# Optimization experiments

Measured on AMD Instinct MI355X. Metric: run time of the kernel, lower is better.

## Reference

```python
import jax, jax.numpy as jnp
import numpy as np

N_HEADS = 12

def setup_inputs() -> dict:
    key = jax.random.key(0)
    ks = jax.random.split(key, 5)
    B, T, H = 8, 1024, 768
    x = jax.random.normal(ks[0], (B, T, H), dtype=jnp.float32)
    # PyTorch Linear init: U(-1/sqrt(fan_in), 1/sqrt(fan_in))
    s1 = 1.0 / np.sqrt(H)
    W_attn = jax.random.uniform(ks[1], (H, 3 * H), minval=-s1, maxval=s1, dtype=jnp.float32)
    b_attn = jax.random.uniform(ks[2], (3 * H,), minval=-s1, maxval=s1, dtype=jnp.float32)
    W_proj = jax.random.uniform(ks[3], (H, H), minval=-s1, maxval=s1, dtype=jnp.float32)
    b_proj = jax.random.uniform(ks[4], (H,), minval=-s1, maxval=s1, dtype=jnp.float32)
    return {"x": x, "W_attn": W_attn, "b_attn": b_attn, "W_proj": W_proj, "b_proj": b_proj}

def reference(x, W_attn, b_attn, W_proj, b_proj):
    B, T, H = x.shape
    nh = N_HEADS
    Hs = H // nh
    qkv = x @ W_attn + b_attn                       # [B,T,3H]
    q, k, v = jnp.split(qkv, 3, axis=-1)            # each [B,T,H]
    # -> [B, nh, T, Hs]
    q = q.reshape(B, T, nh, Hs).transpose(0, 2, 1, 3)
    k = k.reshape(B, T, nh, Hs).transpose(0, 2, 1, 3)
    v = v.reshape(B, T, nh, Hs).transpose(0, 2, 1, 3)
    scale = 1.0 / jnp.sqrt(jnp.asarray(Hs, dtype=x.dtype))
    scores = jnp.einsum("bhqd,bhkd->bhqk", q, k) * scale  # [B,nh,T,T]
    causal = jnp.tril(jnp.ones((T, T), dtype=bool))
    scores = jnp.where(causal, scores, jnp.asarray(-jnp.inf, dtype=scores.dtype))
    attn = jax.nn.softmax(scores, axis=-1)
    out = jnp.einsum("bhqk,bhkd->bhqd", attn, v)    # [B,nh,T,Hs]
    out = out.transpose(0, 2, 1, 3).reshape(B, T, H)
    return out @ W_proj + b_proj
```

## Files before the change

kernel.cpp:

```cpp
#include <hip/hip_runtime.h>
#include <hip/hip_bf16.h>
#include <math.h>


typedef __attribute__((ext_vector_type(4))) float  f32x4;
typedef __attribute__((ext_vector_type(8))) short  bf16x8;
typedef __attribute__((ext_vector_type(4))) short  bf16x4;
typedef __attribute__((ext_vector_type(4))) unsigned int u32x4;

__device__ __forceinline__ unsigned short f2bf(float f) {
    union { float f; unsigned u; } v; v.f = f;
    unsigned r = (v.u + 0x7FFFu + ((v.u >> 16) & 1u)) >> 16;
    return (unsigned short)r;
}

__device__ __forceinline__ bf16x4 pk4(float a, float b, float c, float d) {
    union { struct { __hip_bfloat162 lo, hi; } p; bf16x4 v; } u;
    u.p.lo = __float22bfloat162_rn(make_float2(a, b));
    u.p.hi = __float22bfloat162_rn(make_float2(c, d));
    return u.v;
}

__device__ __forceinline__ void glds16(const unsigned short* g, unsigned short* l) {
    __builtin_amdgcn_global_load_lds((const __attribute__((address_space(1))) void*)g,
                                     (__attribute__((address_space(3))) void*)l, 16, 0, 0);
}

__global__ __launch_bounds__(256)
void cvt_f32_bf16(const float* __restrict__ in, unsigned short* __restrict__ out) {
    const int i = blockIdx.x * 256 + threadIdx.x;
    const float4 v = ((const float4*)in)[i];
    ushort4 o;
    o.x = f2bf(v.x); o.y = f2bf(v.y); o.z = f2bf(v.z); o.w = f2bf(v.w);
    ((ushort4*)out)[i] = o;
}

__global__ __launch_bounds__(256)
void transpose_w(const float* __restrict__ W, unsigned short* __restrict__ Wt,
                 int K, int N) {
    __shared__ float Ts[64][65];
    const int k0 = blockIdx.x * 64, n0 = blockIdx.y * 64;
    const int t = threadIdx.x;
    const int r = t >> 4, cg = (t & 15) * 4;
#pragma unroll
    for (int p = 0; p < 4; ++p) {
        const float4 v = *(const float4*)(&W[(size_t)(k0 + r + p * 16) * N + n0 + cg]);
        Ts[r + p * 16][cg + 0] = v.x;
        Ts[r + p * 16][cg + 1] = v.y;
        Ts[r + p * 16][cg + 2] = v.z;
        Ts[r + p * 16][cg + 3] = v.w;
    }
    __syncthreads();
#pragma unroll
    for (int p = 0; p < 4; ++p) {
        const int n = n0 + r + p * 16;
        ushort4 o;
        o.x = f2bf(Ts[cg + 0][r + p * 16]);
        o.y = f2bf(Ts[cg + 1][r + p * 16]);
        o.z = f2bf(Ts[cg + 2][r + p * 16]);
        o.w = f2bf(Ts[cg + 3][r + p * 16]);
        *(ushort4*)(&Wt[(size_t)n * K + k0 + cg]) = o;
    }
}

template <int MT>
__global__ __launch_bounds__(256)
void gemm_bf16(const unsigned short* __restrict__ A, const unsigned short* __restrict__ Bt,
               const float* __restrict__ bias, void* __restrict__ Cout,
               int M, int N, int K, int out_bf16) {
    __shared__ unsigned short As[MT * 32 * 32];
    __shared__ unsigned short Bs[128 * 32];

    const int t = threadIdx.x;
    const int L = t & 63, w = t >> 6;
    const int l15 = L & 15, quad = L >> 4;
    const int wy = w & 1, wx = w >> 1;
    const int m0 = blockIdx.x * (MT * 32), n0 = blockIdx.y * 128;

    const int srow = t >> 2, koff = (t & 3) * 8;
    const unsigned short* ag = A + (size_t)(m0 + srow) * K + koff;
    const unsigned short* bg = Bt + (size_t)(n0 + srow) * K + koff;
    unsigned short* as0 = As + srow * 32 + koff;
    unsigned short* bs0 = Bs + srow * 32 + koff;
    const size_t gstep = (size_t)64 * K;

    f32x4 acc[MT][4];
#pragma unroll
    for (int mt = 0; mt < MT; ++mt)
#pragma unroll
        for (int nt = 0; nt < 4; ++nt) acc[mt][nt] = (f32x4){0.f, 0.f, 0.f, 0.f};

    for (int k0 = 0; k0 < K; k0 += 32) {
        glds16(ag + k0, as0);
        if (MT == 4) glds16(ag + gstep + k0, as0 + 64 * 32);
        glds16(bg + k0, bs0);
        glds16(bg + gstep + k0, bs0 + 64 * 32);
        __syncthreads();

        bf16x8 af[MT], bfr[4];
#pragma unroll
        for (int mt = 0; mt < MT; ++mt)
            af[mt] = *(const bf16x8*)(As + (wy * (MT * 16) + mt * 16 + l15) * 32 + quad * 8);
#pragma unroll
        for (int nt = 0; nt < 4; ++nt)
            bfr[nt] = *(const bf16x8*)(Bs + (wx * 64 + nt * 16 + l15) * 32 + quad * 8);
#pragma unroll
        for (int mt = 0; mt < MT; ++mt)
#pragma unroll
            for (int nt = 0; nt < 4; ++nt)
                acc[mt][nt] = __builtin_amdgcn_mfma_f32_16x16x32_bf16(af[mt], bfr[nt], acc[mt][nt], 0, 0, 0);
        __syncthreads();
    }

    float bv[4];
#pragma unroll
    for (int nt = 0; nt < 4; ++nt) bv[nt] = bias[n0 + wx * 64 + nt * 16 + l15];
#pragma unroll
    for (int mt = 0; mt < MT; ++mt) {
        const int mrow = m0 + wy * (MT * 16) + mt * 16 + quad * 4;
#pragma unroll
        for (int r = 0; r < 4; ++r) {
            const int m = mrow + r;
            if (out_bf16) {
                unsigned short* C = (unsigned short*)Cout;
#pragma unroll
                for (int nt = 0; nt < 4; ++nt)
                    C[(size_t)m * N + n0 + wx * 64 + nt * 16 + l15] = f2bf(acc[mt][nt][r] + bv[nt]);
            } else {
                float* C = (float*)Cout;
#pragma unroll
                for (int nt = 0; nt < 4; ++nt)
                    C[(size_t)m * N + n0 + wx * 64 + nt * 16 + l15] = acc[mt][nt][r] + bv[nt];
            }
        }
    }
}

__global__ __launch_bounds__(256)
void attn_mfma(const unsigned short* __restrict__ qkv, unsigned short* __restrict__ attb) {
    const int T = 1024, QKVW = 2304, NH = 12, H = 768;
    __shared__ unsigned short Ks[64 * 64];
    __shared__ unsigned short Vt[64 * 72];

    const int t = threadIdx.x;
    const int L = t & 63, w = t >> 6;
    const int l15 = L & 15, quad = L >> 4;
    const int bh = blockIdx.x % 96;
    const int qt = 15 - (int)(blockIdx.x / 96);
    const int h = bh % NH, b = bh / NH;
    const int q0 = qt * 64;

    const unsigned short* base = qkv + (size_t)b * T * QKVW + h * 64;

    const int g0 = t,       r0 = g0 >> 3, lc0 = (g0 & 7) ^ (r0 & 7);
    const int g1 = 256 + t, r1 = g1 >> 3, lc1 = (g1 & 7) ^ (r1 & 7);
    const int vk4 = (t & 15) * 4, vd4 = (t >> 4) * 4;
    const float SM = 0.18033688f;

    glds16(base + (size_t)(q0 + r0) * QKVW + lc0 * 8, Ks + g0 * 8);
    glds16(base + (size_t)(q0 + r1) * QKVW + lc1 * 8, Ks + g1 * 8);
    ushort4 va0, va1, va2, va3;
    {
        const unsigned short* vb = base + 1536 + vd4;
        va0 = *(const ushort4*)(vb + (size_t)(vk4 + 0) * QKVW);
        va1 = *(const ushort4*)(vb + (size_t)(vk4 + 1) * QKVW);
        va2 = *(const ushort4*)(vb + (size_t)(vk4 + 2) * QKVW);
        va3 = *(const ushort4*)(vb + (size_t)(vk4 + 3) * QKVW);
    }
    __syncthreads();

    bf16x8 qf[2];
    {
        const int qrow = 16 * w + l15;
        qf[0] = *(const bf16x8*)(Ks + qrow * 64 + ((quad    ) ^ (qrow & 7)) * 8);
        qf[1] = *(const bf16x8*)(Ks + qrow * 64 + ((quad + 4) ^ (qrow & 7)) * 8);
    }

    f32x4 ot[4];
#pragma unroll
    for (int dt = 0; dt < 4; ++dt) ot[dt] = (f32x4){0.f, 0.f, 0.f, 0.f};
    float mrun = -1e30f, lsum = 0.f;

    for (int j0 = 0; j0 <= q0; j0 += 64) {
        __syncthreads();
        glds16(base + (size_t)(j0 + r0) * QKVW + 768 + lc0 * 8, Ks + g0 * 8);
        glds16(base + (size_t)(j0 + r1) * QKVW + 768 + lc1 * 8, Ks + g1 * 8);
        {
            ushort4 c0, c1, c2, c3;
            c0.x = va0.x; c0.y = va1.x; c0.z = va2.x; c0.w = va3.x;
            c1.x = va0.y; c1.y = va1.y; c1.z = va2.y; c1.w = va3.y;
            c2.x = va0.z; c2.y = va1.z; c2.z = va2.z; c2.w = va3.z;
            c3.x = va0.w; c3.y = va1.w; c3.z = va2.w; c3.w = va3.w;
            *(ushort4*)(Vt + (size_t)(vd4 + 0) * 72 + vk4) = c0;
            *(ushort4*)(Vt + (size_t)(vd4 + 1) * 72 + vk4) = c1;
            *(ushort4*)(Vt + (size_t)(vd4 + 2) * 72 + vk4) = c2;
            *(ushort4*)(Vt + (size_t)(vd4 + 3) * 72 + vk4) = c3;
        }
        if (j0 + 64 <= q0) {
            const unsigned short* vb = base + 1536 + vd4;
            va0 = *(const ushort4*)(vb + (size_t)(j0 + 64 + vk4 + 0) * QKVW);
            va1 = *(const ushort4*)(vb + (size_t)(j0 + 64 + vk4 + 1) * QKVW);
            va2 = *(const ushort4*)(vb + (size_t)(j0 + 64 + vk4 + 2) * QKVW);
            va3 = *(const ushort4*)(vb + (size_t)(j0 + 64 + vk4 + 3) * QKVW);
        }
        __syncthreads();

        f32x4 st[4];
#pragma unroll
        for (int mt = 0; mt < 4; ++mt) {
            st[mt] = (f32x4){0.f, 0.f, 0.f, 0.f};
            const int krow = 16 * mt + l15;
            const bf16x8 kf0 = *(const bf16x8*)(Ks + krow * 64 + ((quad    ) ^ (krow & 7)) * 8);
            const bf16x8 kf1 = *(const bf16x8*)(Ks + krow * 64 + ((quad + 4) ^ (krow & 7)) * 8);
            st[mt] = __builtin_amdgcn_mfma_f32_16x16x32_bf16(kf0, qf[0], st[mt], 0, 0, 0);
            st[mt] = __builtin_amdgcn_mfma_f32_16x16x32_bf16(kf1, qf[1], st[mt], 0, 0, 0);
        }

        if (j0 == q0) {
            const int qin = 16 * w + l15;
#pragma unroll
            for (int mt = 0; mt < 4; ++mt)
#pragma unroll
                for (int r = 0; r < 4; ++r)
                    if (16 * mt + 4 * quad + r > qin) st[mt][r] = -1e30f;
        }

        float nm = st[0][0];
#pragma unroll
        for (int mt = 0; mt < 4; ++mt)
#pragma unroll
            for (int r = 0; r < 4; ++r) nm = fmaxf(nm, st[mt][r]);
        nm = fmaxf(nm, __shfl_xor(nm, 16, 64));
        nm = fmaxf(nm, __shfl_xor(nm, 32, 64));
        const float mnew = fmaxf(mrun, nm);
        const float alpha = __builtin_amdgcn_exp2f((mrun - mnew) * SM);
        float ps[4][4];
        float rs = 0.f;
#pragma unroll
        for (int mt = 0; mt < 4; ++mt)
#pragma unroll
            for (int r = 0; r < 4; ++r) {
                const float p = __builtin_amdgcn_exp2f((st[mt][r] - mnew) * SM);
                ps[mt][r] = p; rs += p;
            }
        rs += __shfl_xor(rs, 16, 64);
        rs += __shfl_xor(rs, 32, 64);
        lsum = lsum * alpha + rs;
        mrun = mnew;
#pragma unroll
        for (int dt = 0; dt < 4; ++dt) {
            ot[dt][0] *= alpha; ot[dt][1] *= alpha; ot[dt][2] *= alpha; ot[dt][3] *= alpha;
        }

        bf16x4 pf[4];
#pragma unroll
        for (int c = 0; c < 4; ++c)
            pf[c] = pk4(ps[c][0], ps[c][1], ps[c][2], ps[c][3]);

#pragma unroll
        for (int c = 0; c < 4; ++c)
#pragma unroll
            for (int dt = 0; dt < 4; ++dt) {
                const bf16x4 vf = *(const bf16x4*)(Vt + (size_t)(16 * dt + l15) * 72 + 16 * c + 4 * quad);
                ot[dt] = __builtin_amdgcn_mfma_f32_16x16x16bf16_1k(vf, pf[c], ot[dt], 0, 0, 0);
            }
    }

    __syncthreads();
    const float inv = 1.0f / lsum;
#pragma unroll
    for (int dt = 0; dt < 4; ++dt)
#pragma unroll
        for (int r = 0; r < 4; ++r)
            Vt[(16 * w + l15) * 72 + 16 * dt + 4 * quad + r] = f2bf(ot[dt][r] * inv);
    __syncthreads();
    {
        const int row = t & 63, hf = t >> 6;
        const u32x4 v0 = *(const u32x4*)(Vt + row * 72 + hf * 16);
        const u32x4 v1 = *(const u32x4*)(Vt + row * 72 + hf * 16 + 8);
        unsigned short* dst = attb + (size_t)(b * T + q0 + row) * H + h * 64 + hf * 16;
        *(u32x4*)dst = v0; *(u32x4*)(dst + 8) = v1;
    }
}

extern "C" void kernel_launch(void* const* d_in, const int* in_sizes, int n_in,
                              void* d_out, int out_size, void* d_ws, size_t ws_size,
                              hipStream_t stream) {
    const float* x      = (const float*)d_in[0];
    const float* W_attn = (const float*)d_in[1];
    const float* b_attn = (const float*)d_in[2];
    const float* W_proj = (const float*)d_in[3];
    const float* b_proj = (const float*)d_in[4];
    float* out = (float*)d_out;

    const int Bn = 8, T = 1024, H = 768, NH = 12;
    const int M = Bn * T;
    const int N1 = 3 * H;

    unsigned short* xb   = (unsigned short*)d_ws;
    unsigned short* Wta  = xb + (size_t)M * H;
    unsigned short* Wtp  = Wta + (size_t)N1 * H;
    unsigned short* qkvb = Wtp + (size_t)H * H;
    unsigned short* attb = qkvb + (size_t)M * N1;

    dim3 blk(256);

    cvt_f32_bf16<<<dim3((M * H) / 1024), blk, 0, stream>>>(x, xb);
    transpose_w<<<dim3(H / 64, N1 / 64), blk, 0, stream>>>(W_attn, Wta, H, N1);
    transpose_w<<<dim3(H / 64, H / 64), blk, 0, stream>>>(W_proj, Wtp, H, H);

    gemm_bf16<4><<<dim3(M / 128, N1 / 128), blk, 0, stream>>>(xb, Wta, b_attn, qkvb, M, N1, H, 1);

    attn_mfma<<<dim3(16 * 96), blk, 0, stream>>>(qkvb, attb);

    gemm_bf16<2><<<dim3(M / 64, H / 128), blk, 0, stream>>>(attb, Wtp, b_proj, out, M, H, H, 0);
}
```

Measured before the change: 197.5 us.

## Merge prep kernels into one launch and XOR-swizzle GEMM LDS tiles

Folds the x conversion and both weight transposes into a single kernel launch that dispatches on block index, removing two launches and their serialization gaps. Separately, the GEMM's shared-memory tiles get an XOR swizzle on the 16-byte chunk index, applied both at global-to-LDS load time and at fragment read time, to reduce LDS bank conflicts. The swizzle adds a little index arithmetic, and the fused prep kernel hardcodes block counts and sizes for this problem shape.

```diff
diff --git a/kernel.cpp b/kernel.cpp
--- a/kernel.cpp
+++ b/kernel.cpp
@@ -27,20 +27,30 @@
 }
 
 __global__ __launch_bounds__(256)
-void cvt_f32_bf16(const float* __restrict__ in, unsigned short* __restrict__ out) {
-    const int i = blockIdx.x * 256 + threadIdx.x;
-    const float4 v = ((const float4*)in)[i];
-    ushort4 o;
-    o.x = f2bf(v.x); o.y = f2bf(v.y); o.z = f2bf(v.z); o.w = f2bf(v.w);
-    ((ushort4*)out)[i] = o;
-}
-
-__global__ __launch_bounds__(256)
-void transpose_w(const float* __restrict__ W, unsigned short* __restrict__ Wt,
-                 int K, int N) {
+void prep_kernel(const float* __restrict__ x, const float* __restrict__ W_attn,
+                 const float* __restrict__ W_proj,
+                 unsigned short* __restrict__ xb, unsigned short* __restrict__ Wta,
+                 unsigned short* __restrict__ Wtp) {
     __shared__ float Ts[64][65];
-    const int k0 = blockIdx.x * 64, n0 = blockIdx.y * 64;
     const int t = threadIdx.x;
+    const int bid = blockIdx.x;
+
+    if (bid < 6144) {
+        const int i = bid * 256 + t;
+        const float4 v = ((const float4*)x)[i];
+        ushort4 o;
+        o.x = f2bf(v.x); o.y = f2bf(v.y); o.z = f2bf(v.z); o.w = f2bf(v.w);
+        ((ushort4*)xb)[i] = o;
+        return;
+    }
+
+    const float* W;
+    unsigned short* Wt;
+    int K, N, b2;
+    if (bid < 6576) { b2 = bid - 6144; W = W_attn; Wt = Wta; K = 768; N = 2304; }
+    else            { b2 = bid - 6576; W = W_proj; Wt = Wtp; K = 768; N = 768;  }
+    const int k0 = (b2 % 12) * 64, n0 = (b2 / 12) * 64;
+
     const int r = t >> 4, cg = (t & 15) * 4;
 #pragma unroll
     for (int p = 0; p < 4; ++p) {
@@ -74,14 +84,17 @@
     const int t = threadIdx.x;
     const int L = t & 63, w = t >> 6;
     const int l15 = L & 15, quad = L >> 4;
+    const int sw = l15 & 3;
     const int wy = w & 1, wx = w >> 1;
     const int m0 = blockIdx.x * (MT * 32), n0 = blockIdx.y * 128;
 
-    const int srow = t >> 2, koff = (t & 3) * 8;
-    const unsigned short* ag = A + (size_t)(m0 + srow) * K + koff;
-    const unsigned short* bg = Bt + (size_t)(n0 + srow) * K + koff;
-    unsigned short* as0 = As + srow * 32 + koff;
-    unsigned short* bs0 = Bs + srow * 32 + koff;
+    const int srow = t >> 2;
+    const int cp = t & 3;
+    const int cl = cp ^ (srow & 3);
+    const unsigned short* ag = A + (size_t)(m0 + srow) * K + cl * 8;
+    const unsigned short* bg = Bt + (size_t)(n0 + srow) * K + cl * 8;
+    unsigned short* as0 = As + srow * 32 + cp * 8;
+    unsigned short* bs0 = Bs + srow * 32 + cp * 8;
     const size_t gstep = (size_t)64 * K;
 
     f32x4 acc[MT][4];
@@ -100,10 +113,10 @@
         bf16x8 af[MT], bfr[4];
 #pragma unroll
         for (int mt = 0; mt < MT; ++mt)
-            af[mt] = *(const bf16x8*)(As + (wy * (MT * 16) + mt * 16 + l15) * 32 + quad * 8);
+            af[mt] = *(const bf16x8*)(As + (wy * (MT * 16) + mt * 16 + l15) * 32 + (quad ^ sw) * 8);
 #pragma unroll
         for (int nt = 0; nt < 4; ++nt)
-            bfr[nt] = *(const bf16x8*)(Bs + (wx * 64 + nt * 16 + l15) * 32 + quad * 8);
+            bfr[nt] = *(const bf16x8*)(Bs + (wx * 64 + nt * 16 + l15) * 32 + (quad ^ sw) * 8);
 #pragma unroll
         for (int mt = 0; mt < MT; ++mt)
 #pragma unroll
@@ -305,9 +318,7 @@
 
     dim3 blk(256);
 
-    cvt_f32_bf16<<<dim3((M * H) / 1024), blk, 0, stream>>>(x, xb);
-    transpose_w<<<dim3(H / 64, N1 / 64), blk, 0, stream>>>(W_attn, Wta, H, N1);
-    transpose_w<<<dim3(H / 64, H / 64), blk, 0, stream>>>(W_proj, Wtp, H, H);
+    prep_kernel<<<dim3(6720), blk, 0, stream>>>(x, W_attn, W_proj, xb, Wta, Wtp);
 
     gemm_bf16<4><<<dim3(M / 128, N1 / 128), blk, 0, stream>>>(xb, Wta, b_attn, qkvb, M, N1, H, 1);
 
```

Measured after the change: 195.3 us. About the same (-1.1%).
